# Kernel tuning notes

Measured on AMD Instinct MI355X. Metric: run time of the kernel, lower is better.

## Reference

```python
import math
import jax, jax.numpy as jnp
import numpy as np

HIDDEN = 2048
HEAD_DIM = 128
NUM_HEADS = 32
NUM_KV_HEADS = 8
GROUP = NUM_HEADS // NUM_KV_HEADS
B, S = 1, 2048


def setup_inputs() -> dict:
    key = jax.random.key(0)
    ks = jax.random.split(key, 9)
    scale_in = 1.0 / math.sqrt(HIDDEN)
    scale_o = 1.0 / math.sqrt(NUM_HEADS * HEAD_DIM)
    x = jax.random.normal(ks[0], (B, S, HIDDEN), dtype=jnp.float32)
    # causal mask (1,1,S,S), int32; masked positions are 0
    mask = jnp.tril(jnp.ones((S, S), dtype=jnp.int32))[None, None]
    wq = jax.random.uniform(ks[1], (HIDDEN, NUM_HEADS * HEAD_DIM), jnp.float32, -scale_in, scale_in)
    bq = jax.random.uniform(ks[2], (NUM_HEADS * HEAD_DIM,), jnp.float32, -scale_in, scale_in)
    wk = jax.random.uniform(ks[3], (HIDDEN, NUM_KV_HEADS * HEAD_DIM), jnp.float32, -scale_in, scale_in)
    bk = jax.random.uniform(ks[4], (NUM_KV_HEADS * HEAD_DIM,), jnp.float32, -scale_in, scale_in)
    wv = jax.random.uniform(ks[5], (HIDDEN, NUM_KV_HEADS * HEAD_DIM), jnp.float32, -scale_in, scale_in)
    bv = jax.random.uniform(ks[6], (NUM_KV_HEADS * HEAD_DIM,), jnp.float32, -scale_in, scale_in)
    wo = jax.random.uniform(ks[7], (NUM_HEADS * HEAD_DIM, HIDDEN), jnp.float32, -scale_o, scale_o)
    bo = jax.random.uniform(ks[8], (HIDDEN,), jnp.float32, -scale_o, scale_o)
    return {"x": x, "mask": mask, "wq": wq, "bq": bq, "wk": wk, "bk": bk,
            "wv": wv, "bv": bv, "wo": wo, "bo": bo}


def reference(x, mask, wq, bq, wk, bk, wv, bv, wo, bo):
    Bb, Ss, _ = x.shape
    inv_sqrt_d = 1.0 / math.sqrt(HEAD_DIM)
    # projections
    q = (x @ wq + bq).reshape(Bb, Ss, NUM_KV_HEADS, GROUP, HEAD_DIM)  # grouped query heads
    k = (x @ wk + bk).reshape(Bb, Ss, NUM_KV_HEADS, HEAD_DIM)
    v = (x @ wv + bv).reshape(Bb, Ss, NUM_KV_HEADS, HEAD_DIM)
    # repeat_interleave(group, dim=2) on k/v == broadcasting each kv head over its
    # GROUP consecutive query heads; einsum avoids the physical KV blow-up.
    scores = jnp.einsum('bqhgd,bshd->bhgqs', q, k) * inv_sqrt_d  # (B, Hkv, G, S, S)
    m = mask[:, :, None]  # (1,1,1,S,S) broadcasts over (Hkv, G)
    scores = jnp.where(m == 0, -jnp.inf, scores)
    attn = jax.nn.softmax(scores, axis=-1)
    out = jnp.einsum('bhgqs,bshd->bqhgd', attn, v).reshape(Bb, Ss, NUM_HEADS * HEAD_DIM)
    return out @ wo + bo
```

## Files before the change

kernel.cpp:

```cpp
#include <hip/hip_runtime.h>

#define HIDDEN 2048
#define S_LEN  2048
#define NH     32
#define NKV    8
#define HD     128
#define QKVN   6144
#define OD     4096

typedef float  f32x4   __attribute__((ext_vector_type(4)));
typedef float  f32x16  __attribute__((ext_vector_type(16)));
typedef __bf16 bf16x8  __attribute__((ext_vector_type(8)));
typedef __bf16 bf16x4  __attribute__((ext_vector_type(4)));
typedef unsigned int u32;

static __device__ __forceinline__ f32x4 mfma16(bf16x8 a, bf16x8 b, f32x4 c) {
  return __builtin_amdgcn_mfma_f32_16x16x32_bf16(a, b, c, 0, 0, 0);
}
static __device__ __forceinline__ f32x16 mfma32(bf16x8 a, bf16x8 b, f32x16 c) {
  return __builtin_amdgcn_mfma_f32_32x32x16_bf16(a, b, c, 0, 0, 0);
}
static __device__ __forceinline__ void gload_lds16(const void* g, void* l) {
  __builtin_amdgcn_global_load_lds(
      (__attribute__((address_space(1))) void*)(g),
      (__attribute__((address_space(3))) void*)(l), 16, 0, 0);
}
static __device__ __forceinline__ u32 pk_bf16(float lo, float hi) {
  u32 r;
  asm("v_cvt_pk_bf16_f32 %0, %1, %2" : "=v"(r) : "v"(lo), "v"(hi));
  return r;
}

__global__ __launch_bounds__(256) void k_cvt(const float* __restrict__ in,
                                             __bf16* __restrict__ out, int n) {
  int i = (blockIdx.x * 256 + threadIdx.x) * 4;
  if (i >= n) return;
  float4 v = *reinterpret_cast<const float4*>(in + i);
  bf16x4 o = {(__bf16)v.x, (__bf16)v.y, (__bf16)v.z, (__bf16)v.w};
  *reinterpret_cast<bf16x4*>(out + i) = o;
}

__global__ __launch_bounds__(256) void k_transpose_cvt(const float* __restrict__ src,
                                                       __bf16* __restrict__ dst,
                                                       int K, int N) {
  __shared__ float tile[32][33];
  int tx = threadIdx.x & 31, ty = threadIdx.x >> 5;
  int n0 = blockIdx.x * 32, k0 = blockIdx.y * 32;
#pragma unroll
  for (int r = 0; r < 4; r++) {
    int k = ty + r * 8;
    tile[k][tx] = src[(size_t)(k0 + k) * N + n0 + tx];
  }
  __syncthreads();
#pragma unroll
  for (int r = 0; r < 4; r++) {
    int n = ty + r * 8;
    dst[(size_t)(n0 + n) * K + k0 + tx] = (__bf16)tile[tx][n];
  }
}

__global__ void k_bias_concat(const float* __restrict__ bq, const float* __restrict__ bk,
                              const float* __restrict__ bv, float* __restrict__ out) {
  int i = blockIdx.x * 256 + threadIdx.x;
  if (i >= QKVN) return;
  out[i] = (i < 4096) ? bq[i] : (i < 5120 ? bk[i - 4096] : bv[i - 5120]);
}

__global__ __launch_bounds__(256) void k_vtrans(const __bf16* __restrict__ qkv,
                                                __bf16* __restrict__ vt) {
  __shared__ __bf16 tile[32][33];
  int tx = threadIdx.x & 31, ty = threadIdx.x >> 5;
  int s0 = blockIdx.x * 32, d0 = blockIdx.y * 32, kv = blockIdx.z;
#pragma unroll
  for (int r = 0; r < 4; r++) {
    int s = ty + r * 8;
    tile[s][tx] = qkv[(size_t)(s0 + s) * QKVN + 5120 + kv * HD + d0 + tx];
  }
  __syncthreads();
#pragma unroll
  for (int r = 0; r < 4; r++) {
    int d = ty + r * 8;
    vt[(size_t)(kv * HD + d0 + d) * S_LEN + s0 + tx] = tile[tx][d];
  }
}

__global__ __launch_bounds__(256, 2) void k_gemm8(const __bf16* __restrict__ A,
                                                  const __bf16* __restrict__ BT,
                                                  const float* __restrict__ bias,
                                                  __bf16* __restrict__ C,
                                                  int M, int N, int K,
                                                  float oscale, int scale_cols) {
  __shared__ __bf16 Al[2][2][4096];
  __shared__ __bf16 Bl[2][2][6144];
  const int tid = threadIdx.x, lane = tid & 63, w = tid >> 6;
  const int l15 = lane & 15, lhi = lane >> 4;
  const int sw = ((blockIdx.x & 7) << 6) + (blockIdx.x >> 3);
  const int mt = sw & 15, nt = sw >> 4;
  const int m0 = mt * 128, n0 = nt * 192;
  const int NKT = K >> 6;
  const __bf16* Ab = A + (size_t)m0 * K;
  const __bf16* Bb = BT + (size_t)n0 * K;

  f32x4 acc[8][3];
#pragma unroll
  for (int i = 0; i < 8; i++)
#pragma unroll
    for (int j = 0; j < 3; j++)
#pragma unroll
      for (int e = 0; e < 4; e++) acc[i][j][e] = 0.f;

#define SGH(buf, kh, ktile)                                                       \
  do {                                                                            \
    _Pragma("unroll") for (int it = 0; it < 2; ++it) {                            \
      int c = it * 256 + tid;                                                     \
      int row = c >> 2, slot = c & 3;                                             \
      int scol = ((slot * 16) ^ (((row >> 1) & 3) << 4)) >> 1;                    \
      gload_lds16(Ab + (size_t)row * K + (ktile) * 64 + (kh) * 32 + scol,         \
                  &Al[buf][kh][c * 8]);                                           \
    }                                                                             \
    _Pragma("unroll") for (int it = 0; it < 3; ++it) {                            \
      int c = it * 256 + tid;                                                     \
      int row = c >> 2, slot = c & 3;                                             \
      int scol = ((slot * 16) ^ (((row >> 1) & 3) << 4)) >> 1;                    \
      gload_lds16(Bb + (size_t)row * K + (ktile) * 64 + (kh) * 32 + scol,         \
                  &Bl[buf][kh][c * 8]);                                           \
    }                                                                             \
  } while (0)

#define RD_AB(cb, kk)                                                             \
  do {                                                                            \
    _Pragma("unroll") for (int i = 0; i < 8; ++i) {                               \
      int row = i * 16 + l15;                                                     \
      af[i] = *(const bf16x8*)(&Al[cb][kk][row * 32 +                             \
                (((lhi * 16) ^ (((row >> 1) & 3) << 4)) >> 1)]);                  \
    }                                                                             \
    _Pragma("unroll") for (int j = 0; j < 3; ++j) {                               \
      int row = w * 48 + j * 16 + l15;                                            \
      bfr[j] = *(const bf16x8*)(&Bl[cb][kk][row * 32 +                            \
                (((lhi * 16) ^ (((row >> 1) & 3) << 4)) >> 1)]);                  \
    }                                                                             \
  } while (0)

#define MFMA24X                                                                   \
  do {                                                                            \
    __builtin_amdgcn_s_setprio(1);                                                \
    _Pragma("unroll") for (int i = 0; i < 8; ++i) {                               \
      _Pragma("unroll") for (int j = 0; j < 3; ++j) {                             \
        acc[i][j] = mfma16(af[i], bfr[j], acc[i][j]);                             \
      }                                                                           \
    }                                                                             \
    __builtin_amdgcn_s_setprio(0);                                                \
  } while (0)

  SGH(0, 0, 0);
  SGH(0, 1, 0);
  asm volatile("s_waitcnt vmcnt(5)" ::: "memory");
  __builtin_amdgcn_s_barrier();
  __builtin_amdgcn_sched_barrier(0);

  for (int kt = 0; kt < NKT; ++kt) {
    const int cb = kt & 1, pb = cb ^ 1;
    const bool pf = (kt + 1 < NKT);
    bf16x8 af[8], bfr[3];

    RD_AB(cb, 0);
    if (pf) SGH(pb, 0, kt + 1);
    __builtin_amdgcn_s_barrier();
    asm volatile("s_waitcnt lgkmcnt(0)" ::: "memory");
    MFMA24X;
    if (pf) {
      asm volatile("s_waitcnt vmcnt(5)" ::: "memory");
    } else {
      asm volatile("s_waitcnt vmcnt(0)" ::: "memory");
    }
    __builtin_amdgcn_s_barrier();
    __builtin_amdgcn_sched_barrier(0);

    RD_AB(cb, 1);
    if (pf) SGH(pb, 1, kt + 1);
    __builtin_amdgcn_s_barrier();
    asm volatile("s_waitcnt lgkmcnt(0)" ::: "memory");
    MFMA24X;
    if (pf) {
      asm volatile("s_waitcnt vmcnt(5)" ::: "memory");
    }
    __builtin_amdgcn_s_barrier();
    __builtin_amdgcn_sched_barrier(0);
  }
#undef SGH
#undef RD_AB
#undef MFMA24X

#pragma unroll
  for (int j = 0; j < 3; j++) {
    int col = n0 + w * 48 + j * 16 + l15;
    float bv = bias[col];
    float sc = (col < scale_cols) ? oscale : 1.0f;
#pragma unroll
    for (int i = 0; i < 8; i++) {
      int r0 = m0 + i * 16 + lhi * 4;
#pragma unroll
      for (int rr = 0; rr < 4; rr++) {
        C[(size_t)(r0 + rr) * N + col] = (__bf16)((acc[i][j][rr] + bv) * sc);
      }
    }
  }
}

__global__ __launch_bounds__(256, 2) void k_gemm_part(const __bf16* __restrict__ A,
                                                      const __bf16* __restrict__ BT,
                                                      float* __restrict__ Cpart,
                                                      int M, int N, int K, int KC) {
  __shared__ __bf16 Al[2][2][4096];
  __shared__ __bf16 Bl[2][2][4096];
  const int tid = threadIdx.x, lane = tid & 63, w = tid >> 6;
  const int l15 = lane & 15, lhi = lane >> 4;
  const int bid = blockIdx.x;
  const int z = bid >> 8, rem = bid & 255;
  const int sw = ((rem & 7) << 5) + (rem >> 3);
  const int mt = sw & 15, nt = sw >> 4;
  const int m0 = mt * 128, n0 = nt * 128;
  const int NKT = KC >> 6;
  const __bf16* Ab = A + (size_t)m0 * K + (size_t)z * KC;
  const __bf16* Bb = BT + (size_t)n0 * K + (size_t)z * KC;

  f32x4 acc[8][2];
#pragma unroll
  for (int i = 0; i < 8; i++)
#pragma unroll
    for (int j = 0; j < 2; j++)
#pragma unroll
      for (int e = 0; e < 4; e++) acc[i][j][e] = 0.f;

#define SGH2(buf, kh, ktile)                                                      \
  do {                                                                            \
    _Pragma("unroll") for (int it = 0; it < 2; ++it) {                            \
      int c = it * 256 + tid;                                                     \
      int row = c >> 2, slot = c & 3;                                             \
      int scol = ((slot * 16) ^ (((row >> 1) & 3) << 4)) >> 1;                    \
      gload_lds16(Ab + (size_t)row * K + (ktile) * 64 + (kh) * 32 + scol,         \
                  &Al[buf][kh][c * 8]);                                           \
    }                                                                             \
    _Pragma("unroll") for (int it = 0; it < 2; ++it) {                            \
      int c = it * 256 + tid;                                                     \
      int row = c >> 2, slot = c & 3;                                             \
      int scol = ((slot * 16) ^ (((row >> 1) & 3) << 4)) >> 1;                    \
      gload_lds16(Bb + (size_t)row * K + (ktile) * 64 + (kh) * 32 + scol,         \
                  &Bl[buf][kh][c * 8]);                                           \
    }                                                                             \
  } while (0)

#define RD_AB2(cb, kk)                                                            \
  do {                                                                            \
    _Pragma("unroll") for (int i = 0; i < 8; ++i) {                               \
      int row = i * 16 + l15;                                                     \
      af[i] = *(const bf16x8*)(&Al[cb][kk][row * 32 +                             \
                (((lhi * 16) ^ (((row >> 1) & 3) << 4)) >> 1)]);                  \
    }                                                                             \
    _Pragma("unroll") for (int j = 0; j < 2; ++j) {                               \
      int row = w * 32 + j * 16 + l15;                                            \
      bfr[j] = *(const bf16x8*)(&Bl[cb][kk][row * 32 +                            \
                (((lhi * 16) ^ (((row >> 1) & 3) << 4)) >> 1)]);                  \
    }                                                                             \
  } while (0)

#define MFMA16X                                                                   \
  do {                                                                            \
    __builtin_amdgcn_s_setprio(1);                                                \
    _Pragma("unroll") for (int i = 0; i < 8; ++i) {                               \
      _Pragma("unroll") for (int j = 0; j < 2; ++j) {                             \
        acc[i][j] = mfma16(af[i], bfr[j], acc[i][j]);                             \
      }                                                                           \
    }                                                                             \
    __builtin_amdgcn_s_setprio(0);                                                \
  } while (0)

  SGH2(0, 0, 0);
  SGH2(0, 1, 0);
  asm volatile("s_waitcnt vmcnt(4)" ::: "memory");
  __builtin_amdgcn_s_barrier();
  __builtin_amdgcn_sched_barrier(0);

  for (int kt = 0; kt < NKT; ++kt) {
    const int cb = kt & 1, pb = cb ^ 1;
    const bool pf = (kt + 1 < NKT);
    bf16x8 af[8], bfr[2];

    RD_AB2(cb, 0);
    if (pf) SGH2(pb, 0, kt + 1);
    __builtin_amdgcn_s_barrier();
    asm volatile("s_waitcnt lgkmcnt(0)" ::: "memory");
    MFMA16X;
    if (pf) {
      asm volatile("s_waitcnt vmcnt(4)" ::: "memory");
    } else {
      asm volatile("s_waitcnt vmcnt(0)" ::: "memory");
    }
    __builtin_amdgcn_s_barrier();
    __builtin_amdgcn_sched_barrier(0);

    RD_AB2(cb, 1);
    if (pf) SGH2(pb, 1, kt + 1);
    __builtin_amdgcn_s_barrier();
    asm volatile("s_waitcnt lgkmcnt(0)" ::: "memory");
    MFMA16X;
    if (pf) {
      asm volatile("s_waitcnt vmcnt(4)" ::: "memory");
    }
    __builtin_amdgcn_s_barrier();
    __builtin_amdgcn_sched_barrier(0);
  }
#undef SGH2
#undef RD_AB2
#undef MFMA16X

  float* C = Cpart + (size_t)z * M * N;
#pragma unroll
  for (int j = 0; j < 2; j++) {
    int col = n0 + w * 32 + j * 16 + l15;
#pragma unroll
    for (int i = 0; i < 8; i++) {
      int r0 = m0 + i * 16 + lhi * 4;
#pragma unroll
      for (int rr = 0; rr < 4; rr++) {
        C[(size_t)(r0 + rr) * N + col] = acc[i][j][rr];
      }
    }
  }
}

__global__ __launch_bounds__(256) void k_ocombine(const float* __restrict__ a,
                                                  const float* __restrict__ b,
                                                  const float* __restrict__ bias,
                                                  float* __restrict__ out) {
  int i = (blockIdx.x * 256 + threadIdx.x) * 4;
  f32x4 va = *(const f32x4*)(a + i);
  f32x4 vb = *(const f32x4*)(b + i);
  f32x4 vbias = *(const f32x4*)(bias + (i & (HIDDEN - 1)));
  f32x4 r = va + vb + vbias;
  *(f32x4*)(out + i) = r;
}

__global__ __launch_bounds__(256, 2) void k_attn(const __bf16* __restrict__ qkv,
                                                 const __bf16* __restrict__ vt,
                                                 __bf16* __restrict__ o) {
  __shared__ __bf16 Kl[2][8192];
  __shared__ __bf16 Vl[2][8192];
  const int tid = threadIdx.x, lane = tid & 63, w = tid >> 6;
  const int l31 = lane & 31, h = lane >> 5;

  const int id = blockIdx.x;
  int tile, head;
  if (id < 256) { head = id >> 4; tile = id & 15; }
  else          { head = 16 + ((id - 256) >> 4); tile = 15 - (id & 15); }
  const int kvh = head >> 2;
  const int qbase = tile * 128 + w * 32;
  const int qg = qbase + l31;
  const int kdiag = (qbase + 31) >> 6;
  const int nkt = 2 * tile + 2;

  bf16x8 qf[8];
  {
    const __bf16* qrow = qkv + (size_t)qg * QKVN + head * HD;
#pragma unroll
    for (int dk = 0; dk < 8; dk++) qf[dk] = *(const bf16x8*)(qrow + dk * 16 + h * 8);
  }

  f32x16 acc[4];
#pragma unroll
  for (int dt = 0; dt < 4; dt++)
#pragma unroll
    for (int r = 0; r < 16; r++) acc[dt][r] = 0.f;
  float m = -INFINITY, lsum = 0.f;

#define STAGE(buf, ktile)                                                           \
  do {                                                                              \
    const int kk0 = (ktile) * 64;                                                   \
    _Pragma("unroll") for (int it = 0; it < 4; it++) {                              \
      int c = it * 256 + tid;                                                       \
      int key = c >> 4, slot = c & 15;                                              \
      int scol = ((slot * 16) ^ ((key & 15) << 4)) >> 1;                            \
      gload_lds16(qkv + (size_t)(kk0 + key) * QKVN + 4096 + kvh * HD + scol,        \
                  &Kl[buf][c * 8]);                                                 \
    }                                                                               \
    _Pragma("unroll") for (int it = 0; it < 4; it++) {                              \
      int c = it * 256 + tid;                                                       \
      int d = c >> 3, slot = c & 7;                                                 \
      int scol = ((slot * 16) ^ ((d & 7) << 4)) >> 1;                               \
      gload_lds16(vt + (size_t)(kvh * HD + d) * S_LEN + kk0 + scol,                 \
                  &Vl[buf][c * 8]);                                                 \
    }                                                                               \
  } while (0)

  STAGE(0, 0);
  __syncthreads();

  for (int kt = 0; kt < nkt; kt++) {
    const int cur = kt & 1;
    if (kt + 1 < nkt) STAGE(cur ^ 1, kt + 1);

    if (kt <= kdiag) {
      const char* Kb = (const char*)&Kl[cur][0];
      const char* Vb = (const char*)&Vl[cur][0];
      const int k0 = kt * 64;
      f32x16 sacc[2];
#pragma unroll
      for (int b = 0; b < 2; b++)
#pragma unroll
        for (int r = 0; r < 16; r++) sacc[b][r] = 0.f;
      __builtin_amdgcn_s_setprio(1);
#pragma unroll
      for (int dk = 0; dk < 8; dk++) {
        const int sA = ((2 * dk + h) ^ (l31 & 15)) * 16;
        bf16x8 kf0 = *(const bf16x8*)(Kb + l31 * 256 + sA);
        bf16x8 kf1 = *(const bf16x8*)(Kb + (32 + l31) * 256 + sA);
        sacc[0] = mfma32(kf0, qf[dk], sacc[0]);
        sacc[1] = mfma32(kf1, qf[dk], sacc[1]);
      }
      __builtin_amdgcn_s_setprio(0);
      float p[32];
#pragma unroll
      for (int b = 0; b < 2; b++)
#pragma unroll
        for (int r = 0; r < 16; r++) p[b * 16 + r] = sacc[b][r];
      if (kt == kdiag) {
#pragma unroll
        for (int b = 0; b < 2; b++)
#pragma unroll
          for (int r = 0; r < 16; r++) {
            int keyg = k0 + b * 32 + (r & 3) + 8 * (r >> 2) + 4 * h;
            if (keyg > qg) p[b * 16 + r] = -INFINITY;
          }
      }
      float t16[16], t8[8], t4[4];
#pragma unroll
      for (int i = 0; i < 16; i++) t16[i] = fmaxf(p[2 * i], p[2 * i + 1]);
#pragma unroll
      for (int i = 0; i < 8; i++) t8[i] = fmaxf(t16[2 * i], t16[2 * i + 1]);
#pragma unroll
      for (int i = 0; i < 4; i++) t4[i] = fmaxf(t8[2 * i], t8[2 * i + 1]);
      float pm = fmaxf(fmaxf(t4[0], t4[1]), fmaxf(t4[2], t4[3]));
      pm = fmaxf(pm, __shfl_xor(pm, 32));
      if (__any(pm - m > 8.f)) {
        float mn = fmaxf(m, pm);
        float corr = __expf(m - mn);
        m = mn;
        lsum *= corr;
#pragma unroll
        for (int dt = 0; dt < 4; dt++)
#pragma unroll
          for (int r = 0; r < 16; r++) acc[dt][r] *= corr;
      }
      float psum = 0.f;
#pragma unroll
      for (int i = 0; i < 32; i++) { p[i] = __expf(p[i] - m); psum += p[i]; }
      lsum += psum;
#pragma unroll
      for (int ks2 = 0; ks2 < 4; ks2++) {
        const int o8 = (ks2 >> 1) * 16 + (ks2 & 1) * 8;
        u32 W0 = pk_bf16(p[o8 + 0], p[o8 + 1]);
        u32 W1 = pk_bf16(p[o8 + 2], p[o8 + 3]);
        u32 W2 = pk_bf16(p[o8 + 4], p[o8 + 5]);
        u32 W3 = pk_bf16(p[o8 + 6], p[o8 + 7]);
        asm("v_permlane32_swap_b32 %0, %1" : "+v"(W0), "+v"(W2));
        asm("v_permlane32_swap_b32 %0, %1" : "+v"(W1), "+v"(W3));
        union { u32 wd[4]; bf16x8 v; } pu;
        pu.wd[0] = W0; pu.wd[1] = W1; pu.wd[2] = W2; pu.wd[3] = W3;
        __builtin_amdgcn_s_setprio(1);
#pragma unroll
        for (int dt = 0; dt < 4; dt++) {
          const int dr = dt * 32 + l31;
          const int sV = ((2 * ks2 + h) ^ (dr & 7)) * 16;
          bf16x8 vf = *(const bf16x8*)(Vb + dr * 128 + sV);
          acc[dt] = mfma32(vf, pu.v, acc[dt]);
        }
        __builtin_amdgcn_s_setprio(0);
      }
    }
    __syncthreads();
  }
#undef STAGE

  lsum += __shfl_xor(lsum, 32);
  const float inv = 1.f / lsum;
  __bf16* orow = o + (size_t)qg * OD + head * HD;
#pragma unroll
  for (int dt = 0; dt < 4; dt++)
#pragma unroll
    for (int rq = 0; rq < 4; rq++) {
      int d = dt * 32 + 8 * rq + 4 * h;
      bf16x4 ov = {(__bf16)(acc[dt][rq * 4 + 0] * inv), (__bf16)(acc[dt][rq * 4 + 1] * inv),
                   (__bf16)(acc[dt][rq * 4 + 2] * inv), (__bf16)(acc[dt][rq * 4 + 3] * inv)};
      *(bf16x4*)(orow + d) = ov;
    }
}

extern "C" void kernel_launch(void* const* d_in, const int* in_sizes, int n_in,
                              void* d_out, int out_size, void* d_ws, size_t ws_size,
                              hipStream_t stream) {
  const float* x  = (const float*)d_in[0];
  const float* wq = (const float*)d_in[2];
  const float* bq = (const float*)d_in[3];
  const float* wk = (const float*)d_in[4];
  const float* bk = (const float*)d_in[5];
  const float* wv = (const float*)d_in[6];
  const float* bv = (const float*)d_in[7];
  const float* wo = (const float*)d_in[8];
  const float* bo = (const float*)d_in[9];
  float* out = (float*)d_out;

  const size_t MB = 1024 * 1024;
  char* ws = (char*)d_ws;
  __bf16* xb    = (__bf16*)(ws);
  __bf16* wqkvT = (__bf16*)(ws + 8 * MB);
  __bf16* woT   = (__bf16*)(ws + 32 * MB);
  __bf16* qkvb  = (__bf16*)(ws + 48 * MB);
  __bf16* vtb   = (__bf16*)(ws + 72 * MB);
  __bf16* ob    = (__bf16*)(ws + 76 * MB);
  float*  bqkv  = (float*)(ws + 92 * MB);
  float*  Cpart = (float*)(ws);

  k_cvt<<<4096, 256, 0, stream>>>(x, xb, HIDDEN * S_LEN);
  k_transpose_cvt<<<dim3(128, 64), 256, 0, stream>>>(wq, wqkvT, HIDDEN, 4096);
  k_transpose_cvt<<<dim3(32, 64), 256, 0, stream>>>(wk, wqkvT + (size_t)4096 * HIDDEN, HIDDEN, 1024);
  k_transpose_cvt<<<dim3(32, 64), 256, 0, stream>>>(wv, wqkvT + (size_t)5120 * HIDDEN, HIDDEN, 1024);
  k_transpose_cvt<<<dim3(64, 128), 256, 0, stream>>>(wo, woT, 4096, HIDDEN);
  k_bias_concat<<<24, 256, 0, stream>>>(bq, bk, bv, bqkv);

  k_gemm8<<<512, 256, 0, stream>>>(xb, wqkvT, bqkv, qkvb, S_LEN, QKVN, HIDDEN,
                                   0.08838834764831845f, 4096);
  k_vtrans<<<dim3(S_LEN / 32, HD / 32, NKV), 256, 0, stream>>>(qkvb, vtb);
  k_attn<<<512, 256, 0, stream>>>(qkvb, vtb, ob);
  k_gemm_part<<<512, 256, 0, stream>>>(ob, woT, Cpart, S_LEN, HIDDEN, OD, OD / 2);
  k_ocombine<<<(S_LEN * HIDDEN) / 1024, 256, 0, stream>>>(
      Cpart, Cpart + (size_t)S_LEN * HIDDEN, bo, out);
}
```

Baseline: 218.2 us.

## Fold log2e into Q scale, use exp2 in softmax, merge QKV weight transposes

The Q scale passed to the QKV GEMM now includes log2(e), so the attention softmax can use exp2f instead of __expf. This removes the extra multiply that __expf performs per score. The row-sum accumulation becomes a tree reduction, which shortens the serial dependency chain. The three separate wq/wk/wv transpose launches are merged into one 3D-grid launch, where blocks beyond the narrower matrices exit early; this cuts launch overhead, but the grid includes idle blocks.

```diff
diff --git a/kernel.cpp b/kernel.cpp
--- a/kernel.cpp
+++ b/kernel.cpp
@@ -38,6 +38,31 @@
   float4 v = *reinterpret_cast<const float4*>(in + i);
   bf16x4 o = {(__bf16)v.x, (__bf16)v.y, (__bf16)v.z, (__bf16)v.w};
   *reinterpret_cast<bf16x4*>(out + i) = o;
+}
+
+__global__ __launch_bounds__(256) void k_transpose_qkv(const float* __restrict__ wq,
+                                                       const float* __restrict__ wk,
+                                                       const float* __restrict__ wv,
+                                                       __bf16* __restrict__ dst) {
+  __shared__ float tile[32][33];
+  const int z = blockIdx.z;
+  const float* src = (z == 0) ? wq : (z == 1 ? wk : wv);
+  const int Nsrc = (z == 0) ? 4096 : 1024;
+  const int coff = (z == 0) ? 0 : (z == 1 ? 4096 : 5120);
+  int tx = threadIdx.x & 31, ty = threadIdx.x >> 5;
+  int n0 = blockIdx.x * 32, k0 = blockIdx.y * 32;
+  if (n0 >= Nsrc) return;
+#pragma unroll
+  for (int r = 0; r < 4; r++) {
+    int k = ty + r * 8;
+    tile[k][tx] = src[(size_t)(k0 + k) * Nsrc + n0 + tx];
+  }
+  __syncthreads();
+#pragma unroll
+  for (int r = 0; r < 4; r++) {
+    int n = ty + r * 8;
+    dst[(size_t)(coff + n0 + n) * HIDDEN + k0 + tx] = (__bf16)tile[tx][n];
+  }
 }
 
 __global__ __launch_bounds__(256) void k_transpose_cvt(const float* __restrict__ src,
@@ -443,7 +468,7 @@
       pm = fmaxf(pm, __shfl_xor(pm, 32));
       if (__any(pm - m > 8.f)) {
         float mn = fmaxf(m, pm);
-        float corr = __expf(m - mn);
+        float corr = exp2f(m - mn);
         m = mn;
         lsum *= corr;
 #pragma unroll
@@ -451,10 +476,16 @@
 #pragma unroll
           for (int r = 0; r < 16; r++) acc[dt][r] *= corr;
       }
-      float psum = 0.f;
-#pragma unroll
-      for (int i = 0; i < 32; i++) { p[i] = __expf(p[i] - m); psum += p[i]; }
-      lsum += psum;
+#pragma unroll
+      for (int i = 0; i < 32; i++) p[i] = exp2f(p[i] - m);
+      float u16[16], u8[8], u4[4];
+#pragma unroll
+      for (int i = 0; i < 16; i++) u16[i] = p[2 * i] + p[2 * i + 1];
+#pragma unroll
+      for (int i = 0; i < 8; i++) u8[i] = u16[2 * i] + u16[2 * i + 1];
+#pragma unroll
+      for (int i = 0; i < 4; i++) u4[i] = u8[2 * i] + u8[2 * i + 1];
+      lsum += (u4[0] + u4[1]) + (u4[2] + u4[3]);
 #pragma unroll
       for (int ks2 = 0; ks2 < 4; ks2++) {
         const int o8 = (ks2 >> 1) * 16 + (ks2 & 1) * 8;
@@ -521,14 +552,12 @@
   float*  Cpart = (float*)(ws);
 
   k_cvt<<<4096, 256, 0, stream>>>(x, xb, HIDDEN * S_LEN);
-  k_transpose_cvt<<<dim3(128, 64), 256, 0, stream>>>(wq, wqkvT, HIDDEN, 4096);
-  k_transpose_cvt<<<dim3(32, 64), 256, 0, stream>>>(wk, wqkvT + (size_t)4096 * HIDDEN, HIDDEN, 1024);
-  k_transpose_cvt<<<dim3(32, 64), 256, 0, stream>>>(wv, wqkvT + (size_t)5120 * HIDDEN, HIDDEN, 1024);
+  k_transpose_qkv<<<dim3(128, 64, 3), 256, 0, stream>>>(wq, wk, wv, wqkvT);
   k_transpose_cvt<<<dim3(64, 128), 256, 0, stream>>>(wo, woT, 4096, HIDDEN);
   k_bias_concat<<<24, 256, 0, stream>>>(bq, bk, bv, bqkv);
 
   k_gemm8<<<512, 256, 0, stream>>>(xb, wqkvT, bqkv, qkvb, S_LEN, QKVN, HIDDEN,
-                                   0.08838834764831845f, 4096);
+                                   0.12751743f, 4096);
   k_vtrans<<<dim3(S_LEN / 32, HD / 32, NKV), 256, 0, stream>>>(qkvb, vtb);
   k_attn<<<512, 256, 0, stream>>>(qkvb, vtb, ob);
   k_gemm_part<<<512, 256, 0, stream>>>(ob, woT, Cpart, S_LEN, HIDDEN, OD, OD / 2);
```

New measurement: 222.5 us. No clear change (+2.0%).
